# Performance work log

Hardware: AMD Instinct MI355X
Metric: run time of the kernel (lower is better)

## Reference

```python
import jax, jax.numpy as jnp
import numpy as np

B, S, E, HEAD = 8, 2048, 512, 64  # head_size = embeddings_dims // no_of_heads = 512 // 8


def setup_inputs() -> dict:
    key = jax.random.key(0)
    kx, kq, kk, kv, kl = jax.random.split(key, 5)
    x = jax.random.normal(kx, (B, S, E), dtype=jnp.float32)
    # Linear(512 -> 64, bias=False); store as [E, HEAD] so y = x @ W
    Wq = jax.random.normal(kq, (E, HEAD), dtype=jnp.float32) * (E ** -0.5)
    Wk = jax.random.normal(kk, (E, HEAD), dtype=jnp.float32) * (E ** -0.5)
    Wv = jax.random.normal(kv, (E, HEAD), dtype=jnp.float32) * (E ** -0.5)
    # Realistic padding mask: 1 for first `length` tokens, 0 after.
    lengths = jax.random.randint(kl, (B,), S // 2, S + 1)
    mask = (jnp.arange(S)[None, :] < lengths[:, None]).astype(jnp.int32)
    return {"x": x, "Wq": Wq, "Wk": Wk, "Wv": Wv, "mask": mask}


def reference(x, Wq, Wk, Wv, mask):
    # q, k, v: [B, S, HEAD]
    q = x @ Wq
    k = x @ Wk
    v = x @ Wv
    # scores: [B, S, S], scaled by head_size**-0.5 (k.shape[-1] in the original)
    scores = jnp.einsum('bqd,bkd->bqk', q, k) * (HEAD ** -0.5)
    causal = jnp.tril(jnp.ones((S, S), dtype=bool))            # [S, S]
    keep = (mask[:, None, :] != 0) & causal[None, :, :]        # padding mask broadcast over query rows, then causal
    scores = jnp.where(keep, scores, -jnp.inf)
    attn = jax.nn.softmax(scores, axis=-1)                     # [B, S, S]
    out = attn @ v                                             # [B, S, HEAD]
    return out
```

## Files before the change

kernel.cpp:

```cpp
#include <hip/hip_runtime.h>

#define BB 8
#define SS 2048
#define EE 512
#define HD 64
#define CHUNK 256
#define KT 64
#define NCH 8
#define PST 72
#define TST 72
#define XRS 40
#define XKB 1280
#define NITEMS 576

typedef __attribute__((ext_vector_type(8))) short bf16x8;
typedef __attribute__((ext_vector_type(4))) float f32x4;

static __device__ __forceinline__ unsigned short f2bf(float f) {
    unsigned u = __builtin_bit_cast(unsigned, f);
    u = (u + 0x7fffu + ((u >> 16) & 1u)) >> 16;
    return (unsigned short)u;
}
static __device__ __forceinline__ unsigned short f2bf_trunc(float f) {
    return (unsigned short)(__builtin_bit_cast(unsigned, f) >> 16);
}
static __device__ __forceinline__ float bf2f(unsigned short h) {
    unsigned u = ((unsigned)h) << 16;
    return __builtin_bit_cast(float, u);
}

__global__ __launch_bounds__(256) void pack_w_kernel(
    const float* __restrict__ Wq, const float* __restrict__ Wk, const float* __restrict__ Wv,
    unsigned short* __restrict__ Wt) {
    int tid = blockIdx.x * 256 + threadIdx.x;
    if (tid >= 3 * EE * HD) return;
    int w_idx = tid / (EE * HD);
    int rem = tid % (EE * HD);
    int kk = rem / HD, n = rem % HD;
    const float* Wsrc = (w_idx == 0) ? Wq : ((w_idx == 1) ? Wk : Wv);
    float val = Wsrc[kk * HD + n];
    if (w_idx == 0) val *= 0.125f;
    int kb = kk >> 5, kr = kk & 31, quad = kr >> 3, j = kr & 7;
    int t = n >> 4, c = n & 15;
    int lane = quad * 16 + c;
    Wt[w_idx * (EE * HD) + ((kb * 4 + t) * 64 + lane) * 8 + j] = f2bf(val);
}

__global__ __launch_bounds__(256) void qkv_kernel(
    const float* __restrict__ x,
    const unsigned short* __restrict__ Wt,
    unsigned short* __restrict__ q,
    unsigned short* __restrict__ k,
    unsigned short* __restrict__ vT) {
    __shared__ __align__(16) unsigned short Xs[16 * XKB];
    const int tid = threadIdx.x;
    const int lane = tid & 63;
    const int t = tid >> 6;
    const int c = lane & 15, quad = lane >> 4;
    const int r0 = blockIdx.x * 32;

    const float* xt = x + (size_t)r0 * EE;
#pragma unroll
    for (int i = 0; i < 16; ++i) {
        int fi = i * 256 + tid;
        int e4 = fi * 4;
        float4 v4 = *(const float4*)(xt + e4);
        int row = e4 >> 9, col = e4 & 511;
        int kb = col >> 5, cc = col & 31;
        ushort4 pk;
        pk.x = f2bf(v4.x); pk.y = f2bf(v4.y); pk.z = f2bf(v4.z); pk.w = f2bf(v4.w);
        *(ushort4*)(&Xs[kb * XKB + row * XRS + cc]) = pk;
    }
    __syncthreads();

    f32x4 acc[2][3];
#pragma unroll
    for (int rt = 0; rt < 2; ++rt)
        for (int m = 0; m < 3; ++m) acc[rt][m] = (f32x4){0.f, 0.f, 0.f, 0.f};

    const unsigned short* wbase0 = Wt + t * 512 + lane * 8;
#pragma unroll
    for (int kb = 0; kb < EE / 32; ++kb) {
        const unsigned short* wb = wbase0 + kb * 2048;
        bf16x8 bfrag[3];
#pragma unroll
        for (int m = 0; m < 3; ++m) bfrag[m] = *(const bf16x8*)(wb + m * (EE * HD));
#pragma unroll
        for (int rt = 0; rt < 2; ++rt) {
            bf16x8 afrag = *(const bf16x8*)(&Xs[kb * XKB + (rt * 16 + c) * XRS + quad * 8]);
#pragma unroll
            for (int m = 0; m < 3; ++m)
                acc[rt][m] = __builtin_amdgcn_mfma_f32_16x16x32_bf16(afrag, bfrag[m], acc[rt][m], 0, 0, 0);
        }
    }

    const int col = t * 16 + c;
#pragma unroll
    for (int rt = 0; rt < 2; ++rt) {
        const int rb = r0 + rt * 16;
        for (int r = 0; r < 4; ++r) {
            int row = rb + quad * 4 + r;
            q[(size_t)row * HD + col] = f2bf(acc[rt][0][r]);
            k[(size_t)row * HD + col] = f2bf(acc[rt][1][r]);
        }
        int row = rb + quad * 4;
        int b_ = row >> 11, sb = row & (SS - 1);
        ushort4 pk;
        pk.x = f2bf(acc[rt][2][0]); pk.y = f2bf(acc[rt][2][1]);
        pk.z = f2bf(acc[rt][2][2]); pk.w = f2bf(acc[rt][2][3]);
        *(ushort4*)(vT + ((size_t)b_ * HD + col) * SS + sb) = pk;
    }
}

__global__ __launch_bounds__(256, 3) void attn_kernel(
    const unsigned short* __restrict__ q,
    const unsigned short* __restrict__ k,
    const unsigned short* __restrict__ vT,
    const int* __restrict__ mask,
    unsigned short* __restrict__ po,
    float* __restrict__ pl,
    float* __restrict__ out) {
    __shared__ __align__(16) unsigned short Ks[2][64 * TST];
    __shared__ __align__(16) unsigned short Vs[2][64 * TST];
    __shared__ __align__(16) unsigned short Ps[4][16 * PST];
    const int tid = threadIdx.x;
    const int lane = tid & 63, wave = tid >> 6;
    const int c = lane & 15, quad = lane >> 4;

    int t = NITEMS - 1 - blockIdx.x;
    const int b_ = t / 72;
    int r = t % 72;
    int g = 0;
    while ((g + 1) * (g + 2) <= r) ++g;
    int rr = r - g * (g + 1);
    const int Q = 2 * g + rr / (g + 1);
    const int cx = rr % (g + 1);
    const int kstart = cx * CHUNK;
    const int kend = min(kstart + CHUNK, Q * 128 + 128);
    const int ntiles = (kend - kstart) >> 6;
    const int nch_active = Q / 2 + 1;
    const int r0 = Q * 128 + wave * 32;

    const unsigned short* qb_p = q + (size_t)b_ * SS * HD;
    const unsigned short* kb_p = k + (size_t)b_ * SS * HD;
    const unsigned short* vb = vT + (size_t)b_ * HD * SS;
    const int* mb = mask + b_ * SS;

    bf16x8 aq[2][2];
#pragma unroll
    for (int rt = 0; rt < 2; ++rt) {
        const unsigned short* qrow = qb_p + (size_t)(r0 + rt * 16 + c) * HD + quad * 8;
        aq[rt][0] = *(const bf16x8*)(qrow);
        aq[rt][1] = *(const bf16x8*)(qrow + 32);
    }

    f32x4 o[2][4];
    float l_i[2][4];
#pragma unroll
    for (int rt = 0; rt < 2; ++rt)
        for (int tt = 0; tt < 4; ++tt) {
            o[rt][tt] = (f32x4){0.f, 0.f, 0.f, 0.f};
            l_i[rt][tt] = 0.f;
        }

    auto stage = [&](int buf, int k0) {
        const unsigned short* ksrc = kb_p + (size_t)k0 * HD;
        unsigned short* kd = &Ks[buf][0];
        unsigned short* vd = &Vs[buf][0];
#pragma unroll
        for (int rnd = 0; rnd < 2; ++rnd) {
            int e = (rnd * 256 + tid) * 8;
            int krow = e >> 6, kcol = e & 63;
            *(bf16x8*)(kd + krow * TST + kcol) = *(const bf16x8*)(ksrc + e);
            int t8 = rnd * 256 + tid;
            int vr = t8 >> 3, vc = (t8 & 7) * 8;
            *(bf16x8*)(vd + vr * TST + vc) = *(const bf16x8*)(vb + (size_t)vr * SS + k0 + vc);
        }
    };

    stage(0, kstart);
    for (int kt = 0; kt < ntiles; ++kt) {
        __syncthreads();
        const unsigned short* ks = &Ks[kt & 1][0];
        const unsigned short* vs = &Vs[kt & 1][0];
        const int k0 = kstart + kt * KT;
        bf16x8 kf[4][2];
#pragma unroll
        for (int kg = 0; kg < 4; ++kg) {
            kf[kg][0] = *(const bf16x8*)(ks + (kg * 16 + c) * TST + quad * 8);
            kf[kg][1] = *(const bf16x8*)(ks + (kg * 16 + c) * TST + 32 + quad * 8);
        }
        if (kt + 1 < ntiles) stage((kt + 1) & 1, k0 + KT);
#pragma unroll
        for (int rt = 0; rt < 2; ++rt) {
            const int rbase = r0 + rt * 16;
            const bool fullc = (k0 + KT <= rbase);
            float p[4][4];
#pragma unroll
            for (int kg = 0; kg < 4; ++kg) {
                f32x4 accs = (f32x4){0.f, 0.f, 0.f, 0.f};
                accs = __builtin_amdgcn_mfma_f32_16x16x32_bf16(aq[rt][0], kf[kg][0], accs, 0, 0, 0);
                accs = __builtin_amdgcn_mfma_f32_16x16x32_bf16(aq[rt][1], kf[kg][1], accs, 0, 0, 0);
                int key = k0 + kg * 16 + c;
                bool mk = (mb[key] != 0);
                for (int rr2 = 0; rr2 < 4; ++rr2) {
                    int row = rbase + quad * 4 + rr2;
                    bool keep = mk && (fullc || key <= row);
                    float e = __expf(fminf(accs[rr2], 80.f));
                    float pe = keep ? e : 0.f;
                    p[kg][rr2] = pe;
                    l_i[rt][rr2] += pe;
                }
            }
            unsigned short* pbuf = &Ps[wave][0];
#pragma unroll
            for (int kg = 0; kg < 4; ++kg)
                for (int rr2 = 0; rr2 < 4; ++rr2)
                    pbuf[(quad * 4 + rr2) * PST + kg * 16 + c] = f2bf_trunc(p[kg][rr2]);
            bf16x8 pa0 = *(const bf16x8*)(pbuf + c * PST + quad * 8);
            bf16x8 pa1 = *(const bf16x8*)(pbuf + c * PST + 32 + quad * 8);
#pragma unroll
            for (int tt = 0; tt < 4; ++tt) {
                bf16x8 bv0 = *(const bf16x8*)(vs + (tt * 16 + c) * TST + quad * 8);
                bf16x8 bv1 = *(const bf16x8*)(vs + (tt * 16 + c) * TST + 32 + quad * 8);
                o[rt][tt] = __builtin_amdgcn_mfma_f32_16x16x32_bf16(pa0, bv0, o[rt][tt], 0, 0, 0);
                o[rt][tt] = __builtin_amdgcn_mfma_f32_16x16x32_bf16(pa1, bv1, o[rt][tt], 0, 0, 0);
            }
        }
    }

#pragma unroll
    for (int rt = 0; rt < 2; ++rt)
        for (int rr2 = 0; rr2 < 4; ++rr2) {
            float s = l_i[rt][rr2];
            s += __shfl_xor(s, 1);
            s += __shfl_xor(s, 2);
            s += __shfl_xor(s, 4);
            s += __shfl_xor(s, 8);
            l_i[rt][rr2] = s;
        }

    if (nch_active == 1) {
#pragma unroll
        for (int rt = 0; rt < 2; ++rt)
            for (int rr2 = 0; rr2 < 4; ++rr2) {
                int row = r0 + rt * 16 + quad * 4 + rr2;
                float l = l_i[rt][rr2];
                float inv = (l > 0.f) ? 1.f / l : 0.f;
                for (int tt = 0; tt < 4; ++tt)
                    out[((size_t)b_ * SS + row) * HD + tt * 16 + c] = o[rt][tt][rr2] * inv;
            }
        return;
    }

#pragma unroll
    for (int rt = 0; rt < 2; ++rt)
        for (int rr2 = 0; rr2 < 4; ++rr2) {
            int row_abs = r0 + rt * 16 + quad * 4 + rr2;
            int qb_i = row_abs >> 6, rl = row_abs & 63;
            size_t base = (size_t)(b_ * 32 + qb_i) * NCH + cx;
            float l = l_i[rt][rr2];
            float inv = (l > 0.f) ? 1.f / l : 0.f;
            for (int tt = 0; tt < 4; ++tt)
                po[base * 4096 + (size_t)rl * 64 + tt * 16 + c] = f2bf(o[rt][tt][rr2] * inv);
            if (c == 0) pl[base * 64 + rl] = l;
        }
}

__global__ __launch_bounds__(256) void combine_kernel(
    const unsigned short* __restrict__ po,
    const float* __restrict__ pl,
    float* __restrict__ out) {
    int t = blockIdx.x * 256 + threadIdx.x;
    if (t >= BB * (SS - 256) * HD) return;
    int d = t & 63;
    int rg = t >> 6;
    int b_ = rg / (SS - 256);
    int row = 256 + rg % (SS - 256);
    int qb = row >> 6, rl = row & 63;
    int nch = row / CHUNK + 1;
    size_t base = (size_t)(b_ * 32 + qb) * NCH;
    float L = 0.f, acc = 0.f;
    for (int c = 0; c < nch; ++c) {
        float l = pl[(base + c) * 64 + rl];
        L += l;
        acc += l * bf2f(po[(base + c) * 4096 + (size_t)rl * 64 + d]);
    }
    out[((size_t)b_ * SS + row) * HD + d] = (L > 0.f) ? acc / L : 0.f;
}

extern "C" void kernel_launch(void* const* d_in, const int* in_sizes, int n_in,
                              void* d_out, int out_size, void* d_ws, size_t ws_size,
                              hipStream_t stream) {
    const float* x = (const float*)d_in[0];
    const float* Wq = (const float*)d_in[1];
    const float* Wk = (const float*)d_in[2];
    const float* Wv = (const float*)d_in[3];
    const int* mask = (const int*)d_in[4];
    float* out = (float*)d_out;

    unsigned short* ws = (unsigned short*)d_ws;
    unsigned short* Wt = ws;
    unsigned short* q = Wt + 3 * EE * HD;
    unsigned short* kk = q + (size_t)BB * SS * HD;
    unsigned short* vT = kk + (size_t)BB * SS * HD;
    unsigned short* po = vT + (size_t)BB * SS * HD;
    float* pl = (float*)(po + (size_t)BB * 32 * NCH * 4096);

    pack_w_kernel<<<dim3((3 * EE * HD + 255) / 256), dim3(256), 0, stream>>>(Wq, Wk, Wv, Wt);
    qkv_kernel<<<dim3(BB * SS / 32), dim3(256), 0, stream>>>(x, Wt, q, kk, vT);
    attn_kernel<<<dim3(NITEMS), dim3(256), 0, stream>>>(q, kk, vT, mask, po, pl, out);
    combine_kernel<<<dim3((BB * (SS - 256) * HD + 255) / 256), dim3(256), 0, stream>>>(po, pl, out);
}
```

Baseline: 114.6 us.

## Split K/V staging into register prefetch and deferred LDS write; batch MFMAs

The attention loop now issues global loads for the next K/V tile into registers at the top of each iteration and writes them to LDS only after the PV matmuls. Before, loads went straight to LDS mid-iteration. The QK and PV MFMA groups are regrouped across both row tiles and wrapped in s_setprio, and the mask loads are hoisted. The combine kernel is vectorised to read 4 bf16 values and write float4 per thread. This raises register pressure and could lower occupancy.

Measured after the change: 109.1 us (median of 2 runs). 4.8% less time.

```diff
diff --git a/kernel.cpp b/kernel.cpp
--- a/kernel.cpp
+++ b/kernel.cpp
@@ -163,70 +163,101 @@
             l_i[rt][tt] = 0.f;
         }
 
-    auto stage = [&](int buf, int k0) {
+    bf16x8 sk[2], sv[2];
+    auto stage_load = [&](int k0) {
         const unsigned short* ksrc = kb_p + (size_t)k0 * HD;
+#pragma unroll
+        for (int rnd = 0; rnd < 2; ++rnd) {
+            int e = (rnd * 256 + tid) * 8;
+            sk[rnd] = *(const bf16x8*)(ksrc + e);
+            int t8 = rnd * 256 + tid;
+            int vr = t8 >> 3, vc = (t8 & 7) * 8;
+            sv[rnd] = *(const bf16x8*)(vb + (size_t)vr * SS + k0 + vc);
+        }
+    };
+    auto stage_write = [&](int buf) {
         unsigned short* kd = &Ks[buf][0];
         unsigned short* vd = &Vs[buf][0];
 #pragma unroll
         for (int rnd = 0; rnd < 2; ++rnd) {
             int e = (rnd * 256 + tid) * 8;
             int krow = e >> 6, kcol = e & 63;
-            *(bf16x8*)(kd + krow * TST + kcol) = *(const bf16x8*)(ksrc + e);
+            *(bf16x8*)(kd + krow * TST + kcol) = sk[rnd];
             int t8 = rnd * 256 + tid;
             int vr = t8 >> 3, vc = (t8 & 7) * 8;
-            *(bf16x8*)(vd + vr * TST + vc) = *(const bf16x8*)(vb + (size_t)vr * SS + k0 + vc);
+            *(bf16x8*)(vd + vr * TST + vc) = sv[rnd];
         }
     };
 
-    stage(0, kstart);
+    stage_load(kstart);
+    stage_write(0);
     for (int kt = 0; kt < ntiles; ++kt) {
         __syncthreads();
+        const int k0 = kstart + kt * KT;
+        const bool pre = (kt + 1 < ntiles);
+        if (pre) stage_load(k0 + KT);
         const unsigned short* ks = &Ks[kt & 1][0];
         const unsigned short* vs = &Vs[kt & 1][0];
-        const int k0 = kstart + kt * KT;
+
+        bool mk4[4];
+#pragma unroll
+        for (int kg = 0; kg < 4; ++kg) mk4[kg] = (mb[k0 + kg * 16 + c] != 0);
+
         bf16x8 kf[4][2];
 #pragma unroll
         for (int kg = 0; kg < 4; ++kg) {
             kf[kg][0] = *(const bf16x8*)(ks + (kg * 16 + c) * TST + quad * 8);
             kf[kg][1] = *(const bf16x8*)(ks + (kg * 16 + c) * TST + 32 + quad * 8);
         }
-        if (kt + 1 < ntiles) stage((kt + 1) & 1, k0 + KT);
+
+        bf16x8 pa[2][2];
 #pragma unroll
         for (int rt = 0; rt < 2; ++rt) {
             const int rbase = r0 + rt * 16;
             const bool fullc = (k0 + KT <= rbase);
-            float p[4][4];
+            f32x4 accs4[4];
+            __builtin_amdgcn_s_setprio(1);
 #pragma unroll
             for (int kg = 0; kg < 4; ++kg) {
-                f32x4 accs = (f32x4){0.f, 0.f, 0.f, 0.f};
-                accs = __builtin_amdgcn_mfma_f32_16x16x32_bf16(aq[rt][0], kf[kg][0], accs, 0, 0, 0);
-                accs = __builtin_amdgcn_mfma_f32_16x16x32_bf16(aq[rt][1], kf[kg][1], accs, 0, 0, 0);
+                f32x4 a = (f32x4){0.f, 0.f, 0.f, 0.f};
+                a = __builtin_amdgcn_mfma_f32_16x16x32_bf16(aq[rt][0], kf[kg][0], a, 0, 0, 0);
+                a = __builtin_amdgcn_mfma_f32_16x16x32_bf16(aq[rt][1], kf[kg][1], a, 0, 0, 0);
+                accs4[kg] = a;
+            }
+            __builtin_amdgcn_s_setprio(0);
+            unsigned short* pbuf = &Ps[wave][0];
+#pragma unroll
+            for (int kg = 0; kg < 4; ++kg) {
                 int key = k0 + kg * 16 + c;
-                bool mk = (mb[key] != 0);
+                bool mk = mk4[kg];
+#pragma unroll
                 for (int rr2 = 0; rr2 < 4; ++rr2) {
                     int row = rbase + quad * 4 + rr2;
                     bool keep = mk && (fullc || key <= row);
-                    float e = __expf(fminf(accs[rr2], 80.f));
+                    float e = __expf(fminf(accs4[kg][rr2], 80.f));
                     float pe = keep ? e : 0.f;
-                    p[kg][rr2] = pe;
                     l_i[rt][rr2] += pe;
+                    pbuf[(quad * 4 + rr2) * PST + kg * 16 + c] = f2bf_trunc(pe);
                 }
             }
-            unsigned short* pbuf = &Ps[wave][0];
-#pragma unroll
-            for (int kg = 0; kg < 4; ++kg)
-                for (int rr2 = 0; rr2 < 4; ++rr2)
-                    pbuf[(quad * 4 + rr2) * PST + kg * 16 + c] = f2bf_trunc(p[kg][rr2]);
-            bf16x8 pa0 = *(const bf16x8*)(pbuf + c * PST + quad * 8);
-            bf16x8 pa1 = *(const bf16x8*)(pbuf + c * PST + 32 + quad * 8);
-#pragma unroll
-            for (int tt = 0; tt < 4; ++tt) {
-                bf16x8 bv0 = *(const bf16x8*)(vs + (tt * 16 + c) * TST + quad * 8);
-                bf16x8 bv1 = *(const bf16x8*)(vs + (tt * 16 + c) * TST + 32 + quad * 8);
-                o[rt][tt] = __builtin_amdgcn_mfma_f32_16x16x32_bf16(pa0, bv0, o[rt][tt], 0, 0, 0);
-                o[rt][tt] = __builtin_amdgcn_mfma_f32_16x16x32_bf16(pa1, bv1, o[rt][tt], 0, 0, 0);
+            pa[rt][0] = *(const bf16x8*)(pbuf + c * PST + quad * 8);
+            pa[rt][1] = *(const bf16x8*)(pbuf + c * PST + 32 + quad * 8);
+        }
+
+#pragma unroll
+        for (int tt = 0; tt < 4; ++tt) {
+            bf16x8 bv0 = *(const bf16x8*)(vs + (tt * 16 + c) * TST + quad * 8);
+            bf16x8 bv1 = *(const bf16x8*)(vs + (tt * 16 + c) * TST + 32 + quad * 8);
+            __builtin_amdgcn_s_setprio(1);
+#pragma unroll
+            for (int rt = 0; rt < 2; ++rt) {
+                o[rt][tt] = __builtin_amdgcn_mfma_f32_16x16x32_bf16(pa[rt][0], bv0, o[rt][tt], 0, 0, 0);
+                o[rt][tt] = __builtin_amdgcn_mfma_f32_16x16x32_bf16(pa[rt][1], bv1, o[rt][tt], 0, 0, 0);
             }
-        }
+            __builtin_amdgcn_s_setprio(0);
+        }
+
+        if (pre) stage_write((kt + 1) & 1);
     }
 
 #pragma unroll
@@ -272,21 +303,29 @@
     const float* __restrict__ pl,
     float* __restrict__ out) {
     int t = blockIdx.x * 256 + threadIdx.x;
-    if (t >= BB * (SS - 256) * HD) return;
-    int d = t & 63;
-    int rg = t >> 6;
+    if (t >= BB * (SS - 256) * (HD / 4)) return;
+    int d4 = (t & 15) * 4;
+    int rg = t >> 4;
     int b_ = rg / (SS - 256);
     int row = 256 + rg % (SS - 256);
     int qb = row >> 6, rl = row & 63;
     int nch = row / CHUNK + 1;
     size_t base = (size_t)(b_ * 32 + qb) * NCH;
-    float L = 0.f, acc = 0.f;
-    for (int c = 0; c < nch; ++c) {
-        float l = pl[(base + c) * 64 + rl];
+    float L = 0.f;
+    float acc0 = 0.f, acc1 = 0.f, acc2 = 0.f, acc3 = 0.f;
+    for (int cc = 0; cc < nch; ++cc) {
+        float l = pl[(base + cc) * 64 + rl];
         L += l;
-        acc += l * bf2f(po[(base + c) * 4096 + (size_t)rl * 64 + d]);
-    }
-    out[((size_t)b_ * SS + row) * HD + d] = (L > 0.f) ? acc / L : 0.f;
+        ushort4 pk = *(const ushort4*)(po + (base + cc) * 4096 + (size_t)rl * 64 + d4);
+        acc0 += l * bf2f(pk.x);
+        acc1 += l * bf2f(pk.y);
+        acc2 += l * bf2f(pk.z);
+        acc3 += l * bf2f(pk.w);
+    }
+    float inv = (L > 0.f) ? 1.f / L : 0.f;
+    float4 o4;
+    o4.x = acc0 * inv; o4.y = acc1 * inv; o4.z = acc2 * inv; o4.w = acc3 * inv;
+    *(float4*)(out + ((size_t)b_ * SS + row) * HD + d4) = o4;
 }
 
 extern "C" void kernel_launch(void* const* d_in, const int* in_sizes, int n_in,
@@ -310,5 +349,5 @@
     pack_w_kernel<<<dim3((3 * EE * HD + 255) / 256), dim3(256), 0, stream>>>(Wq, Wk, Wv, Wt);
     qkv_kernel<<<dim3(BB * SS / 32), dim3(256), 0, stream>>>(x, Wt, q, kk, vT);
     attn_kernel<<<dim3(NITEMS), dim3(256), 0, stream>>>(q, kk, vT, mask, po, pl, out);
-    combine_kernel<<<dim3((BB * (SS - 256) * HD + 255) / 256), dim3(256), 0, stream>>>(po, pl, out);
-}
+    combine_kernel<<<dim3((BB * (SS - 256) * (HD / 4) + 255) / 256), dim3(256), 0, stream>>>(po, pl, out);
+}
```
